# Performance work log

Measured on AMD Instinct MI355X. Metric: run time of the kernel, lower is better.

The kernel has to match this reference:

```python
import jax, jax.numpy as jnp
import numpy as np

N_NODES = 10000
DROP_P = 0.5


def _gcn_conv(x, row, col, W, b):
    # PyG GCNConv: add self-loops, symmetric normalization, scatter-add aggregate
    n = x.shape[0]
    loops = jnp.arange(n)
    row = jnp.concatenate([row, loops])  # src
    col = jnp.concatenate([col, loops])  # dst
    xw = x @ W  # [N, H]
    deg = jax.ops.segment_sum(jnp.ones(col.shape, dtype=xw.dtype), col, num_segments=n)
    dinv = jnp.where(deg > 0, jax.lax.rsqrt(jnp.maximum(deg, 1e-12)), 0.0)
    norm = dinv[row] * dinv[col]  # [E+N]
    msg = xw[row] * norm[:, None]  # [E+N, H]
    return jax.ops.segment_sum(msg, col, num_segments=n) + b


def setup_inputs() -> dict:
    key = jax.random.key(0)
    k1, k2, k3, k4, k5, k6 = jax.random.split(key, 6)
    B, N, E, F, H = 8, N_NODES, 320000, 128, 128
    xs = jax.random.normal(k1, (B, N, F), dtype=jnp.float32)
    edge_indexs = jax.random.randint(k2, (B, 2, E), 0, N, dtype=jnp.int64)
    s1 = 1.0 / np.sqrt(F)
    s2 = 1.0 / np.sqrt(H)
    W1 = jax.random.uniform(k3, (F, H), jnp.float32, -s1, s1)
    b1 = jnp.zeros((H,), jnp.float32)
    W2 = jax.random.uniform(k4, (H, H), jnp.float32, -s2, s2)
    b2 = jnp.zeros((H,), jnp.float32)
    return {"xs": xs, "edge_indexs": edge_indexs, "W1": W1, "b1": b1, "W2": W2, "b2": b2}


def reference(xs, edge_indexs, W1, b1, W2, b2):
    # Fixed dropout mask (F.dropout is active in the original; fixed key for determinism)
    drop_mask = jax.random.bernoulli(jax.random.key(42), 1.0 - DROP_P, (xs.shape[1], W1.shape[1]))

    def per_graph(x, ei):
        row, col = ei[0], ei[1]
        h = jax.nn.relu(_gcn_conv(x, row, col, W1, b1))
        h = jnp.where(drop_mask, h / (1.0 - DROP_P), 0.0)
        return _gcn_conv(h, row, col, W2, b2)

    return jax.vmap(per_graph)(xs, edge_indexs)
```

## Files before the change

kernel.cpp:

```cpp
#include <hip/hip_runtime.h>
#include <hip/hip_bf16.h>

#define NB 8
#define NN 10000
#define NE 320000
#define NF 128
#define NH 128
#define RNG 32
#define RS 313
#define BCAP 12288
#define P1E 8000
#define P1CAP 512

typedef __attribute__((ext_vector_type(8))) _Float16 half8;
typedef __attribute__((ext_vector_type(4))) float f32x4;


__device__ __forceinline__ int load_edge_nt(const int* ei, size_t idx, int is64) {
    if (is64) return (int)__builtin_nontemporal_load(((const long long*)ei) + idx);
    return __builtin_nontemporal_load(ei + idx);
}

__device__ __forceinline__ unsigned short f2bf(float x) {
    __hip_bfloat16 h = __float2bfloat16(x);
    return *reinterpret_cast<unsigned short*>(&h);
}

__device__ __forceinline__ void bf8_add(float* a, uint4 u) {
    union { unsigned q; float f; } t;
    t.q = u.x << 16;         a[0] += t.f;
    t.q = u.x & 0xffff0000u; a[1] += t.f;
    t.q = u.y << 16;         a[2] += t.f;
    t.q = u.y & 0xffff0000u; a[3] += t.f;
    t.q = u.z << 16;         a[4] += t.f;
    t.q = u.z & 0xffff0000u; a[5] += t.f;
    t.q = u.w << 16;         a[6] += t.f;
    t.q = u.w & 0xffff0000u; a[7] += t.f;
}

__global__ void detect_kernel(const int* __restrict__ ei, int* __restrict__ flag) {
    __shared__ int s;
    if (threadIdx.x == 0) s = 1;
    __syncthreads();
    int bad = 0;
    for (int q = threadIdx.x; q < 1024; q += 256)
        if (ei[2 * q + 1] != 0) bad = 1;
    if (bad) atomicAnd(&s, 0);
    __syncthreads();
    if (threadIdx.x == 0) *flag = s;
}

__global__ void mask_kernel(float* __restrict__ mask) {
    const unsigned TOT = NN * NH;
    unsigned i = blockIdx.x * 256 + threadIdx.x;
    if (i >= TOT) return;
    const unsigned ks0 = 0u, ks1 = 42u, ks2 = 0x1BD11BDAu ^ 0u ^ 42u;
    unsigned x0 = 0u + ks0;
    unsigned x1 = i + ks1;
#define TFR(r) { x0 += x1; x1 = (x1 << (r)) | (x1 >> (32 - (r))); x1 ^= x0; }
    TFR(13) TFR(15) TFR(26) TFR(6)
    x0 += ks1; x1 += ks2 + 1u;
    TFR(17) TFR(29) TFR(16) TFR(24)
    x0 += ks2; x1 += ks0 + 2u;
    TFR(13) TFR(15) TFR(26) TFR(6)
    x0 += ks0; x1 += ks1 + 3u;
    TFR(17) TFR(29) TFR(16) TFR(24)
    x0 += ks1; x1 += ks2 + 4u;
    TFR(13) TFR(15) TFR(26) TFR(6)
    x0 += ks2; x1 += ks0 + 5u;
#undef TFR
    unsigned bits = x0 ^ x1;
    mask[i] = (bits & 0x80000000u) ? 0.0f : 2.0f;
}

__global__ __launch_bounds__(256) void part_kernel(const int* __restrict__ ei,
                                                   const int* __restrict__ flag,
                                                   int* __restrict__ gcur,
                                                   unsigned* __restrict__ gbucket) {
    int b = blockIdx.x & 7;
    int chunk = blockIdx.x >> 3;
    int e0 = chunk * P1E, e1 = e0 + P1E;
    __shared__ int bcnt[RNG];
    __shared__ unsigned bbuf[RNG][P1CAP];
    for (int i = threadIdx.x; i < RNG; i += 256) bcnt[i] = 0;
    __syncthreads();
    int is64 = *flag;
    size_t base = (size_t)b * 2 * NE;
    for (int e = e0 + threadIdx.x; e < e1; e += 256) {
        int row = load_edge_nt(ei, base + e, is64);
        int col = load_edge_nt(ei, base + NE + e, is64);
        int bk = col / RS;
        unsigned pk = ((unsigned)col << 14) | (unsigned)row;
        int p = atomicAdd(&bcnt[bk], 1);
        if (p < P1CAP) bbuf[bk][p] = pk;
        else {
            int gp = atomicAdd(&gcur[b * RNG + bk], 1);
            if (gp < BCAP) gbucket[(size_t)(b * RNG + bk) * BCAP + gp] = pk;
        }
    }
    __syncthreads();
    int wave = threadIdx.x >> 6, lane = threadIdx.x & 63;
    for (int bk = wave; bk < RNG; bk += 4) {
        int len = bcnt[bk]; if (len > P1CAP) len = P1CAP;
        int gb = 0;
        if (lane == 0) gb = atomicAdd(&gcur[b * RNG + bk], len);
        gb = __shfl(gb, 0);
        unsigned* dst = gbucket + (size_t)(b * RNG + bk) * BCAP;
        for (int i = lane; i < len; i += 64)
            if (gb + i < BCAP) dst[gb + i] = bbuf[bk][i];
    }
}

__global__ __launch_bounds__(512) void build_kernel(const unsigned* __restrict__ gbucket,
                                                    const int* __restrict__ gcur,
                                                    int* __restrict__ csr,
                                                    int* __restrict__ deg,
                                                    int* __restrict__ offs) {
    int b = blockIdx.x & 7;
    int r = blockIdx.x >> 3;
    int n0 = r * RS;
    int nloc = (NN - n0 < RS) ? (NN - n0) : RS;
    __shared__ int cnt[512];
    __shared__ int cur[RS];
    __shared__ int buf[BCAP];
    int gidx = b * RNG + r;
    int K = gcur[gidx]; if (K > BCAP) K = BCAP;
    const unsigned* src = gbucket + (size_t)gidx * BCAP;
    int t = threadIdx.x;
    cnt[t] = 0;
    __syncthreads();
    for (int i = t; i < K; i += 512)
        atomicAdd(&cnt[(src[i] >> 14) - n0], 1);
    __syncthreads();
    int v = cnt[t];
    __syncthreads();
    int x = v;
    cnt[t] = x;
    __syncthreads();
    for (int off = 1; off < 512; off <<= 1) {
        int add = (t >= off) ? cnt[t - off] : 0;
        __syncthreads();
        x += add;
        cnt[t] = x;
        __syncthreads();
    }
    int excl = x - v;
    if (t < nloc) {
        deg[b * NN + n0 + t] = v;
        offs[b * NN + n0 + t] = gidx * BCAP + excl;
        cur[t] = excl;
    }
    __syncthreads();
    for (int i = t; i < K; i += 512) {
        unsigned pk = src[i];
        int p = atomicAdd(&cur[(pk >> 14) - n0], 1);
        buf[p] = (int)((pk & 16383u) << 8);
    }
    __syncthreads();
    int* dstc = csr + (size_t)gidx * BCAP;
    for (int i = t; i < K; i += 512) dstc[i] = buf[i];
}

__global__ __launch_bounds__(256) void dinv_kernel(const int* __restrict__ deg,
                                                   float* __restrict__ dinv) {
    int i = blockIdx.x * 256 + threadIdx.x;
    if (i >= NB * NN) return;
    dinv[i] = 1.0f / sqrtf((float)(deg[i] + 1));
}

__global__ __launch_bounds__(256) void gemm_mfma(const float* __restrict__ X,
                                                 const float* __restrict__ Wm,
                                                 const float* __restrict__ dinv,
                                                 unsigned short* __restrict__ y) {
    __shared__ _Float16 WT[128][136];
    int b = blockIdx.x & 7;
    int row0 = (blockIdx.x >> 3) * 64;
    int t = threadIdx.x;
    for (int e = t; e < 16384; e += 256) {
        int k = e >> 7, c = e & 127;
        WT[c][k] = (_Float16)Wm[e];
    }
    __syncthreads();

    int lane = t & 63;
    int wrow = row0 + (t >> 6) * 16;
    int r = lane & 15;
    int g = lane >> 4;
    const float* Xb = X + (size_t)b * NN * NF;
    int grow = wrow + r;

    f32x4 acc[8] = {};
#pragma unroll
    for (int kk = 0; kk < 4; ++kk) {
        half8 a;
        if (grow < NN) {
            const float* px = Xb + (size_t)grow * NF + kk * 32 + g * 8;
            float4 x0 = *(const float4*)px;
            float4 x1 = *(const float4*)(px + 4);
            a[0] = (_Float16)x0.x; a[1] = (_Float16)x0.y;
            a[2] = (_Float16)x0.z; a[3] = (_Float16)x0.w;
            a[4] = (_Float16)x1.x; a[5] = (_Float16)x1.y;
            a[6] = (_Float16)x1.z; a[7] = (_Float16)x1.w;
        } else {
            a = (half8)(_Float16)0.0f;
        }
#pragma unroll
        for (int c = 0; c < 8; ++c) {
            half8 bf = *(const half8*)&WT[c * 16 + r][kk * 32 + g * 8];
            acc[c] = __builtin_amdgcn_mfma_f32_16x16x32_f16(a, bf, acc[c], 0, 0, 0);
        }
    }

#pragma unroll
    for (int i = 0; i < 4; ++i) {
        int orow = wrow + g * 4 + i;
        if (orow >= NN) continue;
        float d = dinv[b * NN + orow];
        unsigned short* yp = y + ((size_t)b * NN + orow) * NH + r;
#pragma unroll
        for (int c = 0; c < 8; ++c)
            yp[c * 16] = f2bf(acc[c][i] * d);
    }
}

template<int LAYER>
__global__ __launch_bounds__(256) void aggregate_full(const unsigned short* __restrict__ y,
                                                      const int* __restrict__ offs,
                                                      const int* __restrict__ deg,
                                                      const int* __restrict__ csr,
                                                      const float* __restrict__ dinv,
                                                      const float* __restrict__ bias,
                                                      const float* __restrict__ mask,
                                                      float* __restrict__ out) {
    int b = blockIdx.x & 7;
    int w = threadIdx.x >> 6;
    int idx = (blockIdx.x >> 3) * 4 + w;
    int n0 = idx, n1 = idx + 5000;
    int lane = threadIdx.x & 63;
    int q = lane >> 4;
    unsigned q16 = (unsigned)(lane & 15) * 16u;
    const char* ybc = (const char*)(y + (size_t)b * NN * NH);

    float a0[8] = {0.f,0.f,0.f,0.f,0.f,0.f,0.f,0.f};
    float a1[8] = {0.f,0.f,0.f,0.f,0.f,0.f,0.f,0.f};
    if (q == 0) {
        uint4 s0 = *(const uint4*)(ybc + (unsigned)n0 * 256u + q16);
        uint4 s1 = *(const uint4*)(ybc + (unsigned)n1 * 256u + q16);
        bf8_add(a0, s0);
        bf8_add(a1, s1);
    }

    const int* ob = offs + b * NN;
    const int* db = deg + b * NN;
    int ba = ob[n0], o1a = ba + db[n0];
    int bb = ob[n1], o1b = bb + db[n1];

#define PROCQ(r_, j_, acc_) { \
    unsigned o = (unsigned)__shfl((r_), (j_) + q); \
    uint4 u = *(const uint4*)(ybc + o + q16); \
    bf8_add(acc_, u); \
}
#define PROCT(r_, j_, rem_, acc_) { \
    unsigned o = (unsigned)__shfl((r_), (j_) + (q < (rem_) ? q : 0)); \
    uint4 u = *(const uint4*)(ybc + o + q16); \
    if (q < (rem_)) bf8_add(acc_, u); \
}

    while (ba < o1a || bb < o1b) {
        int ma = o1a - ba; ma = ma < 0 ? 0 : (ma > 64 ? 64 : ma);
        int mb = o1b - bb; mb = mb < 0 ? 0 : (mb > 64 ? 64 : mb);
        int ra = (lane < ma) ? csr[ba + lane] : 0;
        int rb = (lane < mb) ? csr[bb + lane] : 0;
        int mmin = ma < mb ? ma : mb;
        int jj = 0;
#pragma unroll 2
        for (; jj + 3 < mmin; jj += 4) {
            PROCQ(ra, jj, a0)
            PROCQ(rb, jj, a1)
        }
        int ja = jj, jb = jj;
#pragma unroll 2
        for (; ja + 3 < ma; ja += 4) PROCQ(ra, ja, a0)
        if (ja < ma) PROCT(ra, ja, ma - ja, a0)
#pragma unroll 2
        for (; jb + 3 < mb; jb += 4) PROCQ(rb, jb, a1)
        if (jb < mb) PROCT(rb, jb, mb - jb, a1)
        ba += 64; bb += 64;
    }
#undef PROCQ
#undef PROCT

#pragma unroll
    for (int i = 0; i < 8; ++i) {
        a0[i] += __shfl_xor(a0[i], 16);
        a0[i] += __shfl_xor(a0[i], 32);
        a1[i] += __shfl_xor(a1[i], 16);
        a1[i] += __shfl_xor(a1[i], 32);
    }

    if (q < 2) {
        int n = q ? n1 : n0;
        float av[8];
#pragma unroll
        for (int i = 0; i < 8; ++i) av[i] = q ? a1[i] : a0[i];
        float d = dinv[b * NN + n];
        unsigned f0 = (lane & 15) * 8;
        float4 bi0 = *(const float4*)(bias + f0);
        float4 bi1 = *(const float4*)(bias + f0 + 4);
        float4 o0, o1;
        o0.x = fmaf(d, av[0], bi0.x);
        o0.y = fmaf(d, av[1], bi0.y);
        o0.z = fmaf(d, av[2], bi0.z);
        o0.w = fmaf(d, av[3], bi0.w);
        o1.x = fmaf(d, av[4], bi1.x);
        o1.y = fmaf(d, av[5], bi1.y);
        o1.z = fmaf(d, av[6], bi1.z);
        o1.w = fmaf(d, av[7], bi1.w);
        if (LAYER == 1) {
            float4 m0 = *(const float4*)(mask + (size_t)n * NH + f0);
            float4 m1 = *(const float4*)(mask + (size_t)n * NH + f0 + 4);
            o0.x = fmaxf(o0.x, 0.f) * m0.x;
            o0.y = fmaxf(o0.y, 0.f) * m0.y;
            o0.z = fmaxf(o0.z, 0.f) * m0.z;
            o0.w = fmaxf(o0.w, 0.f) * m0.w;
            o1.x = fmaxf(o1.x, 0.f) * m1.x;
            o1.y = fmaxf(o1.y, 0.f) * m1.y;
            o1.z = fmaxf(o1.z, 0.f) * m1.z;
            o1.w = fmaxf(o1.w, 0.f) * m1.w;
        }
        float* op = out + ((size_t)b * NN + n) * NH + f0;
        *(float4*)op = o0;
        *(float4*)(op + 4) = o1;
    }
}

extern "C" void kernel_launch(void* const* d_in, const int* in_sizes, int n_in,
                              void* d_out, int out_size, void* d_ws, size_t ws_size,
                              hipStream_t stream) {
    const float* xs = (const float*)d_in[0];
    const int*   ei = (const int*)d_in[1];
    const float* W1 = (const float*)d_in[2];
    const float* b1 = (const float*)d_in[3];
    const float* W2 = (const float*)d_in[4];
    const float* b2 = (const float*)d_in[5];
    float* out = (float*)d_out;

    float* ws        = (float*)d_ws;
    float* dinv      = ws;
    int*   deg       = (int*)(ws + 80000);
    int*   flag      = (int*)(ws + 160000);
    float* mask      = ws + 160016;
    int*   offs      = (int*)(ws + 1440016);
    int*   gcur      = (int*)(ws + 1520016);
    unsigned* gbucket= (unsigned*)(ws + 1520272);
    int*   csr       = (int*)(ws + 4666000);
    unsigned short* y= (unsigned short*)(ws + 7811728);

    hipMemsetAsync(gcur, 0, NB * RNG * sizeof(int), stream);
    detect_kernel<<<1, 256, 0, stream>>>(ei, flag);
    mask_kernel<<<(NN * NH + 255) / 256, 256, 0, stream>>>(mask);
    part_kernel<<<8 * (NE / P1E), 256, 0, stream>>>(ei, flag, gcur, gbucket);
    build_kernel<<<NB * RNG, 512, 0, stream>>>(gbucket, gcur, csr, deg, offs);
    dinv_kernel<<<(NB * NN + 255) / 256, 256, 0, stream>>>(deg, dinv);

    dim3 gemm_grid(8 * ((NN + 63) / 64));
    dim3 agg_grid(NB * (5000 / 4));

    gemm_mfma<<<gemm_grid, 256, 0, stream>>>(xs, W1, dinv, y);
    aggregate_full<1><<<agg_grid, 256, 0, stream>>>(y, offs, deg, csr, dinv, b1, mask, out);

    gemm_mfma<<<gemm_grid, 256, 0, stream>>>(out, W2, dinv, y);
    aggregate_full<2><<<agg_grid, 256, 0, stream>>>(y, offs, deg, csr, dinv, b2, nullptr, out);
}
```

Baseline: 209.3 us.

## Aggregate four nodes per wave, fold dinv into build, drop memset, shrink partition chunks

```diff
diff --git a/kernel.cpp b/kernel.cpp
--- a/kernel.cpp
+++ b/kernel.cpp
@@ -9,8 +9,8 @@
 #define RNG 32
 #define RS 313
 #define BCAP 12288
-#define P1E 8000
-#define P1CAP 512
+#define P1E 2500
+#define P1CAP 192
 
 typedef __attribute__((ext_vector_type(8))) _Float16 half8;
 typedef __attribute__((ext_vector_type(4))) float f32x4;
@@ -38,9 +38,11 @@
     t.q = u.w & 0xffff0000u; a[7] += t.f;
 }
 
-__global__ void detect_kernel(const int* __restrict__ ei, int* __restrict__ flag) {
+__global__ void detect_kernel(const int* __restrict__ ei, int* __restrict__ flag,
+                              int* __restrict__ gcur) {
     __shared__ int s;
     if (threadIdx.x == 0) s = 1;
+    if (threadIdx.x < NB * RNG) gcur[threadIdx.x] = 0;
     __syncthreads();
     int bad = 0;
     for (int q = threadIdx.x; q < 1024; q += 256)
@@ -82,7 +84,7 @@
     int e0 = chunk * P1E, e1 = e0 + P1E;
     __shared__ int bcnt[RNG];
     __shared__ unsigned bbuf[RNG][P1CAP];
-    for (int i = threadIdx.x; i < RNG; i += 256) bcnt[i] = 0;
+    if (threadIdx.x < RNG) bcnt[threadIdx.x] = 0;
     __syncthreads();
     int is64 = *flag;
     size_t base = (size_t)b * 2 * NE;
@@ -115,7 +117,8 @@
                                                     const int* __restrict__ gcur,
                                                     int* __restrict__ csr,
                                                     int* __restrict__ deg,
-                                                    int* __restrict__ offs) {
+                                                    int* __restrict__ offs,
+                                                    float* __restrict__ dinv) {
     int b = blockIdx.x & 7;
     int r = blockIdx.x >> 3;
     int n0 = r * RS;
@@ -148,6 +151,7 @@
     if (t < nloc) {
         deg[b * NN + n0 + t] = v;
         offs[b * NN + n0 + t] = gidx * BCAP + excl;
+        dinv[b * NN + n0 + t] = 1.0f / sqrtf((float)(v + 1));
         cur[t] = excl;
     }
     __syncthreads();
@@ -159,13 +163,6 @@
     __syncthreads();
     int* dstc = csr + (size_t)gidx * BCAP;
     for (int i = t; i < K; i += 512) dstc[i] = buf[i];
-}
-
-__global__ __launch_bounds__(256) void dinv_kernel(const int* __restrict__ deg,
-                                                   float* __restrict__ dinv) {
-    int i = blockIdx.x * 256 + threadIdx.x;
-    if (i >= NB * NN) return;
-    dinv[i] = 1.0f / sqrtf((float)(deg[i] + 1));
 }
 
 __global__ __launch_bounds__(256) void gemm_mfma(const float* __restrict__ X,
@@ -235,25 +232,27 @@
     int b = blockIdx.x & 7;
     int w = threadIdx.x >> 6;
     int idx = (blockIdx.x >> 3) * 4 + w;
-    int n0 = idx, n1 = idx + 5000;
+    int n0 = idx, n1 = idx + 2500, n2 = idx + 5000, n3 = idx + 7500;
     int lane = threadIdx.x & 63;
     int q = lane >> 4;
     unsigned q16 = (unsigned)(lane & 15) * 16u;
     const char* ybc = (const char*)(y + (size_t)b * NN * NH);
 
-    float a0[8] = {0.f,0.f,0.f,0.f,0.f,0.f,0.f,0.f};
-    float a1[8] = {0.f,0.f,0.f,0.f,0.f,0.f,0.f,0.f};
+    float a0[8] = {}; float a1[8] = {}; float a2[8] = {}; float a3[8] = {};
     if (q == 0) {
         uint4 s0 = *(const uint4*)(ybc + (unsigned)n0 * 256u + q16);
         uint4 s1 = *(const uint4*)(ybc + (unsigned)n1 * 256u + q16);
-        bf8_add(a0, s0);
-        bf8_add(a1, s1);
+        uint4 s2 = *(const uint4*)(ybc + (unsigned)n2 * 256u + q16);
+        uint4 s3 = *(const uint4*)(ybc + (unsigned)n3 * 256u + q16);
+        bf8_add(a0, s0); bf8_add(a1, s1); bf8_add(a2, s2); bf8_add(a3, s3);
     }
 
     const int* ob = offs + b * NN;
     const int* db = deg + b * NN;
-    int ba = ob[n0], o1a = ba + db[n0];
-    int bb = ob[n1], o1b = bb + db[n1];
+    int b0 = ob[n0], e0 = b0 + db[n0];
+    int b1 = ob[n1], e1 = b1 + db[n1];
+    int b2 = ob[n2], e2 = b2 + db[n2];
+    int b3 = ob[n3], e3 = b3 + db[n3];
 
 #define PROCQ(r_, j_, acc_) { \
     unsigned o = (unsigned)__shfl((r_), (j_) + q); \
@@ -266,72 +265,84 @@
     if (q < (rem_)) bf8_add(acc_, u); \
 }
 
-    while (ba < o1a || bb < o1b) {
-        int ma = o1a - ba; ma = ma < 0 ? 0 : (ma > 64 ? 64 : ma);
-        int mb = o1b - bb; mb = mb < 0 ? 0 : (mb > 64 ? 64 : mb);
-        int ra = (lane < ma) ? csr[ba + lane] : 0;
-        int rb = (lane < mb) ? csr[bb + lane] : 0;
-        int mmin = ma < mb ? ma : mb;
+    while (b0 < e0 || b1 < e1 || b2 < e2 || b3 < e3) {
+        int m0 = e0 - b0; m0 = m0 < 0 ? 0 : (m0 > 64 ? 64 : m0);
+        int m1 = e1 - b1; m1 = m1 < 0 ? 0 : (m1 > 64 ? 64 : m1);
+        int m2 = e2 - b2; m2 = m2 < 0 ? 0 : (m2 > 64 ? 64 : m2);
+        int m3 = e3 - b3; m3 = m3 < 0 ? 0 : (m3 > 64 ? 64 : m3);
+        int r0 = (lane < m0) ? csr[b0 + lane] : 0;
+        int r1 = (lane < m1) ? csr[b1 + lane] : 0;
+        int r2 = (lane < m2) ? csr[b2 + lane] : 0;
+        int r3 = (lane < m3) ? csr[b3 + lane] : 0;
+        int mmin = m0 < m1 ? m0 : m1;
+        mmin = mmin < m2 ? mmin : m2;
+        mmin = mmin < m3 ? mmin : m3;
         int jj = 0;
+        for (; jj + 3 < mmin; jj += 4) {
+            PROCQ(r0, jj, a0)
+            PROCQ(r1, jj, a1)
+            PROCQ(r2, jj, a2)
+            PROCQ(r3, jj, a3)
+        }
+        int j0 = jj, j1 = jj, j2 = jj, j3 = jj;
 #pragma unroll 2
-        for (; jj + 3 < mmin; jj += 4) {
-            PROCQ(ra, jj, a0)
-            PROCQ(rb, jj, a1)
-        }
-        int ja = jj, jb = jj;
+        for (; j0 + 3 < m0; j0 += 4) PROCQ(r0, j0, a0)
+        if (j0 < m0) PROCT(r0, j0, m0 - j0, a0)
 #pragma unroll 2
-        for (; ja + 3 < ma; ja += 4) PROCQ(ra, ja, a0)
-        if (ja < ma) PROCT(ra, ja, ma - ja, a0)
+        for (; j1 + 3 < m1; j1 += 4) PROCQ(r1, j1, a1)
+        if (j1 < m1) PROCT(r1, j1, m1 - j1, a1)
 #pragma unroll 2
-        for (; jb + 3 < mb; jb += 4) PROCQ(rb, jb, a1)
-        if (jb < mb) PROCT(rb, jb, mb - jb, a1)
-        ba += 64; bb += 64;
+        for (; j2 + 3 < m2; j2 += 4) PROCQ(r2, j2, a2)
+        if (j2 < m2) PROCT(r2, j2, m2 - j2, a2)
+#pragma unroll 2
+        for (; j3 + 3 < m3; j3 += 4) PROCQ(r3, j3, a3)
+        if (j3 < m3) PROCT(r3, j3, m3 - j3, a3)
+        b0 += 64; b1 += 64; b2 += 64; b3 += 64;
     }
 #undef PROCQ
 #undef PROCT
 
 #pragma unroll
     for (int i = 0; i < 8; ++i) {
-        a0[i] += __shfl_xor(a0[i], 16);
-        a0[i] += __shfl_xor(a0[i], 32);
-        a1[i] += __shfl_xor(a1[i], 16);
-        a1[i] += __shfl_xor(a1[i], 32);
-    }
-
-    if (q < 2) {
-        int n = q ? n1 : n0;
-        float av[8];
-#pragma unroll
-        for (int i = 0; i < 8; ++i) av[i] = q ? a1[i] : a0[i];
-        float d = dinv[b * NN + n];
-        unsigned f0 = (lane & 15) * 8;
-        float4 bi0 = *(const float4*)(bias + f0);
-        float4 bi1 = *(const float4*)(bias + f0 + 4);
-        float4 o0, o1;
-        o0.x = fmaf(d, av[0], bi0.x);
-        o0.y = fmaf(d, av[1], bi0.y);
-        o0.z = fmaf(d, av[2], bi0.z);
-        o0.w = fmaf(d, av[3], bi0.w);
-        o1.x = fmaf(d, av[4], bi1.x);
-        o1.y = fmaf(d, av[5], bi1.y);
-        o1.z = fmaf(d, av[6], bi1.z);
-        o1.w = fmaf(d, av[7], bi1.w);
-        if (LAYER == 1) {
-            float4 m0 = *(const float4*)(mask + (size_t)n * NH + f0);
-            float4 m1 = *(const float4*)(mask + (size_t)n * NH + f0 + 4);
-            o0.x = fmaxf(o0.x, 0.f) * m0.x;
-            o0.y = fmaxf(o0.y, 0.f) * m0.y;
-            o0.z = fmaxf(o0.z, 0.f) * m0.z;
-            o0.w = fmaxf(o0.w, 0.f) * m0.w;
-            o1.x = fmaxf(o1.x, 0.f) * m1.x;
-            o1.y = fmaxf(o1.y, 0.f) * m1.y;
-            o1.z = fmaxf(o1.z, 0.f) * m1.z;
-            o1.w = fmaxf(o1.w, 0.f) * m1.w;
-        }
-        float* op = out + ((size_t)b * NN + n) * NH + f0;
-        *(float4*)op = o0;
-        *(float4*)(op + 4) = o1;
-    }
+        a0[i] += __shfl_xor(a0[i], 16); a0[i] += __shfl_xor(a0[i], 32);
+        a1[i] += __shfl_xor(a1[i], 16); a1[i] += __shfl_xor(a1[i], 32);
+        a2[i] += __shfl_xor(a2[i], 16); a2[i] += __shfl_xor(a2[i], 32);
+        a3[i] += __shfl_xor(a3[i], 16); a3[i] += __shfl_xor(a3[i], 32);
+    }
+
+    int n = (q == 0) ? n0 : (q == 1) ? n1 : (q == 2) ? n2 : n3;
+    float av[8];
+#pragma unroll
+    for (int i = 0; i < 8; ++i)
+        av[i] = (q == 0) ? a0[i] : (q == 1) ? a1[i] : (q == 2) ? a2[i] : a3[i];
+    float d = dinv[b * NN + n];
+    unsigned f0 = (lane & 15) * 8;
+    float4 bi0 = *(const float4*)(bias + f0);
+    float4 bi1 = *(const float4*)(bias + f0 + 4);
+    float4 o0, o1;
+    o0.x = fmaf(d, av[0], bi0.x);
+    o0.y = fmaf(d, av[1], bi0.y);
+    o0.z = fmaf(d, av[2], bi0.z);
+    o0.w = fmaf(d, av[3], bi0.w);
+    o1.x = fmaf(d, av[4], bi1.x);
+    o1.y = fmaf(d, av[5], bi1.y);
+    o1.z = fmaf(d, av[6], bi1.z);
+    o1.w = fmaf(d, av[7], bi1.w);
+    if (LAYER == 1) {
+        float4 m0 = *(const float4*)(mask + (size_t)n * NH + f0);
+        float4 m1 = *(const float4*)(mask + (size_t)n * NH + f0 + 4);
+        o0.x = fmaxf(o0.x, 0.f) * m0.x;
+        o0.y = fmaxf(o0.y, 0.f) * m0.y;
+        o0.z = fmaxf(o0.z, 0.f) * m0.z;
+        o0.w = fmaxf(o0.w, 0.f) * m0.w;
+        o1.x = fmaxf(o1.x, 0.f) * m1.x;
+        o1.y = fmaxf(o1.y, 0.f) * m1.y;
+        o1.z = fmaxf(o1.z, 0.f) * m1.z;
+        o1.w = fmaxf(o1.w, 0.f) * m1.w;
+    }
+    float* op = out + ((size_t)b * NN + n) * NH + f0;
+    *(float4*)op = o0;
+    *(float4*)(op + 4) = o1;
 }
 
 extern "C" void kernel_launch(void* const* d_in, const int* in_sizes, int n_in,
@@ -356,15 +367,13 @@
     int*   csr       = (int*)(ws + 4666000);
     unsigned short* y= (unsigned short*)(ws + 7811728);
 
-    hipMemsetAsync(gcur, 0, NB * RNG * sizeof(int), stream);
-    detect_kernel<<<1, 256, 0, stream>>>(ei, flag);
+    detect_kernel<<<1, 256, 0, stream>>>(ei, flag, gcur);
     mask_kernel<<<(NN * NH + 255) / 256, 256, 0, stream>>>(mask);
     part_kernel<<<8 * (NE / P1E), 256, 0, stream>>>(ei, flag, gcur, gbucket);
-    build_kernel<<<NB * RNG, 512, 0, stream>>>(gbucket, gcur, csr, deg, offs);
-    dinv_kernel<<<(NB * NN + 255) / 256, 256, 0, stream>>>(deg, dinv);
+    build_kernel<<<NB * RNG, 512, 0, stream>>>(gbucket, gcur, csr, deg, offs, dinv);
 
     dim3 gemm_grid(8 * ((NN + 63) / 64));
-    dim3 agg_grid(NB * (5000 / 4));
+    dim3 agg_grid(NB * (2500 / 4));
 
     gemm_mfma<<<gemm_grid, 256, 0, stream>>>(xs, W1, dinv, y);
     aggregate_full<1><<<agg_grid, 256, 0, stream>>>(y, offs, deg, csr, dinv, b1, mask, out);
```

After: 241.9 us. 15.5% more time.
